# Kernel optimization log

Hardware: AMD Instinct MI355X
Metric: run time of the kernel (lower is better)

Reference implementation:

```python
import jax, jax.numpy as jnp
import numpy as np

HEAD_DIM = 128
N_HEADS = 16
N_KV_HEADS = 4
N_REP = N_HEADS // N_KV_HEADS


def _rope(x, cos, sin):
    # x: [B, S, Hk, D]; cos/sin: [S, D/2]
    xr = x.reshape(*x.shape[:-1], -1, 2)
    x0, x1 = xr[..., 0], xr[..., 1]
    c = cos[None, :, None, :]
    s = sin[None, :, None, :]
    o0 = x0 * c - x1 * s
    o1 = x0 * s + x1 * c
    return jnp.stack([o0, o1], axis=-1).reshape(x.shape)


def setup_inputs() -> dict:
    key = jax.random.key(0)
    ks = jax.random.split(key, 7)
    B, S, DIM = 2, 1024, 2048
    KV_DIM = HEAD_DIM * N_KV_HEADS
    x = jax.random.normal(ks[0], (B, S, DIM), dtype=jnp.float32)
    # rotary angles like LLaMA: freqs = 1/10000^(2i/D)
    inv_freq = 1.0 / (10000.0 ** (np.arange(0, HEAD_DIM, 2, dtype=np.float32) / HEAD_DIM))
    ang = np.arange(S, dtype=np.float32)[:, None] * inv_freq[None, :]  # [S, D/2]
    theta_cos = jnp.asarray(np.cos(ang))
    theta_sin = jnp.asarray(np.sin(ang))
    sc = 0.02
    wq = jax.random.normal(ks[1], (DIM, DIM), dtype=jnp.float32) * sc
    wk = jax.random.normal(ks[2], (DIM, KV_DIM), dtype=jnp.float32) * sc
    wv = jax.random.normal(ks[3], (DIM, KV_DIM), dtype=jnp.float32) * sc
    wo = jax.random.normal(ks[4], (DIM, DIM), dtype=jnp.float32) * sc
    return {"x": x, "theta_cos": theta_cos, "theta_sin": theta_sin,
            "wq": wq, "wk": wk, "wv": wv, "wo": wo}


def reference(x, theta_cos, theta_sin, wq, wk, wv, wo):
    B, S, DIM = x.shape
    # projections
    xq = (x @ wq).reshape(B, S, N_HEADS, HEAD_DIM).transpose(0, 2, 1, 3)  # [B,H,S,D]
    xk = (x @ wk).reshape(B, S, N_KV_HEADS, HEAD_DIM)                      # [B,S,Hk,D]
    xv = (x @ wv).reshape(B, S, N_KV_HEADS, HEAD_DIM)
    # RoPE on K and V only (faithful to source: Q is NOT rotated)
    xk = _rope(xk, theta_cos, theta_sin)
    xv = _rope(xv, theta_cos, theta_sin)
    # GQA repeat: [B,S,Hk,D] -> [B,H,S,D] (each kv head repeated consecutively)
    xk = jnp.repeat(xk.transpose(0, 2, 1, 3), N_REP, axis=1)
    xv = jnp.repeat(xv.transpose(0, 2, 1, 3), N_REP, axis=1)
    scale = HEAD_DIM ** (-0.5)
    att = jnp.einsum('bhqd,bhkd->bhqk', xq, xk) * scale
    # faithful masking: tril then masked_fill(att == 0, -inf)
    tri = jnp.tril(jnp.ones((S, S), dtype=bool))
    att = jnp.where(tri[None, None], att, 0.0)
    att = jnp.where(att == 0.0, -jnp.inf, att)
    att = jax.nn.softmax(att, axis=-1)
    y = jnp.einsum('bhqk,bhkd->bhqd', att, xv)
    out = y.transpose(0, 2, 1, 3).reshape(B, S, DIM)
    return out @ wo
```

## Files before the change

kernel.cpp:

```cpp
#include <hip/hip_runtime.h>
#include <hip/hip_bf16.h>
#include <stdint.h>
#include <math.h>

typedef _Float16 half_t;
typedef __attribute__((ext_vector_type(2))) _Float16 h2_t;
typedef __attribute__((ext_vector_type(4))) _Float16 h4_t;
typedef __attribute__((ext_vector_type(8))) _Float16 h8_t;
typedef __attribute__((ext_vector_type(4))) float f32x4;

#if __has_builtin(__builtin_amdgcn_exp2f)
#define EXP2(x) __builtin_amdgcn_exp2f(x)
#else
#define EXP2(x) exp2f(x)
#endif

__device__ __forceinline__ void gload16(const void* g, void* l) {
    __builtin_amdgcn_global_load_lds(
        (const __attribute__((address_space(1))) uint32_t*)(uintptr_t)g,
        (__attribute__((address_space(3))) uint32_t*)(uint32_t)(uintptr_t)l,
        16, 0, 0);
}

__global__ __launch_bounds__(256) void prep(const float* __restrict__ x, half_t* __restrict__ xh,
                                            const float* __restrict__ wq, const float* __restrict__ wk,
                                            const float* __restrict__ wv, const float* __restrict__ wo,
                                            half_t* __restrict__ qt, half_t* __restrict__ kt,
                                            half_t* __restrict__ vt, half_t* __restrict__ ot) {
    __shared__ half_t T[32][36];
    const int bx = blockIdx.x;
    if (bx < 2048) {
        int g = (bx * 256 + threadIdx.x) * 8;
        float4 a = *(const float4*)(x + g);
        float4 b = *(const float4*)(x + g + 4);
        h8_t o = {(half_t)a.x,(half_t)a.y,(half_t)a.z,(half_t)a.w,
                  (half_t)b.x,(half_t)b.y,(half_t)b.z,(half_t)b.w};
        *(h8_t*)(xh + g) = o;
        return;
    }
    const int wb = bx - 2048;
    const float* src; half_t* dst; int Nd, t;
    if (wb < 4096)      { src = wq; dst = qt; Nd = 2048; t = wb; }
    else if (wb < 5120) { src = wk; dst = kt; Nd = 512;  t = wb - 4096; }
    else if (wb < 6144) { src = wv; dst = vt; Nd = 512;  t = wb - 5120; }
    else                { src = wo; dst = ot; Nd = 2048; t = wb - 6144; }
    const int K = 2048;
    int nt = Nd >> 5;
    int ti = t / nt, tj = t % nt;
    int r  = threadIdx.x >> 3;
    int c4 = (threadIdx.x & 7) << 2;
    float4 v = *(const float4*)(src + (size_t)(ti*32 + r) * Nd + tj*32 + c4);
    T[r][c4+0] = (half_t)v.x; T[r][c4+1] = (half_t)v.y;
    T[r][c4+2] = (half_t)v.z; T[r][c4+3] = (half_t)v.w;
    __syncthreads();
    h4_t o = {T[c4+0][r], T[c4+1][r], T[c4+2][r], T[c4+3][r]};
    *(h4_t*)(dst + (size_t)(tj*32 + r) * K + ti*32 + c4) = o;
}

template<int BM, int QKV, typename CT>
__global__ __launch_bounds__(256) void gemm_t(const half_t* __restrict__ A,
                                              const half_t* __restrict__ Bq,
                                              const half_t* __restrict__ Bk,
                                              const half_t* __restrict__ Bv,
                                              CT* __restrict__ Cq,
                                              half_t* __restrict__ Ck,
                                              half_t* __restrict__ Cv,
                                              int NB, int K) {
    constexpr int MI  = BM / 32;
    constexpr int ACH = BM / 8;
    constexpr int TOT = ACH + 16;
    constexpr int PW  = TOT / 4;
    __shared__ half_t Ah[BM * 64];
    __shared__ half_t Bh[128 * 64];
    const int tid = threadIdx.x, lane = tid & 63, wid = tid >> 6;
    const int lr = lane & 15, lg = lane >> 4;
    const int wm = wid >> 1, wn = wid & 1;
    const int nwg = gridDim.x, bid = blockIdx.x;
    const int swz = (bid & 7) * (nwg >> 3) + (bid >> 3);
    const int bm = swz / NB, bn = swz % NB;
    const int m0 = bm * BM;

    const half_t* W; CT* Cc; int cs, col0;
    if constexpr (QKV) {
        if (bn < 16)      { W = Bq + (size_t)bn * 128 * K;        Cc = Cq;       cs = 2048; col0 = bn * 128; }
        else if (bn < 20) { W = Bk + (size_t)(bn - 16) * 128 * K; Cc = (CT*)Ck;  cs = 512;  col0 = (bn - 16) * 128; }
        else              { W = Bv + (size_t)(bn - 20) * 128 * K; Cc = (CT*)Cv;  cs = 512;  col0 = (bn - 20) * 128; }
    } else {
        W = Bq + (size_t)bn * 128 * K; Cc = Cq; cs = NB * 128; col0 = bn * 128;
    }

    const half_t* Arow = A + (size_t)m0 * K;
    f32x4 acc[MI][4] = {};

    for (int k0 = 0; k0 < K; k0 += 64) {
        #pragma unroll
        for (int c = 0; c < PW; c++) {
            const int chunk = wid * PW + c;
            const int o = lane * 16;
            if (chunk < ACH) {
                const int go   = (chunk << 10) + o;
                const int row  = go >> 7;
                const int colb = (go & 127) ^ ((row & 7) << 4);
                gload16(Arow + (size_t)row * K + k0 + (colb >> 1), (char*)Ah + (chunk << 10));
            } else {
                const int go   = ((chunk - ACH) << 10) + o;
                const int row  = go >> 7;
                const int colb = (go & 127) ^ ((row & 7) << 4);
                gload16(W + (size_t)row * K + k0 + (colb >> 1), (char*)Bh + ((chunk - ACH) << 10));
            }
        }
        __syncthreads();
        h8_t af[2][MI], bf[2][4];
        #pragma unroll
        for (int kk = 0; kk < 2; kk++) {
            #pragma unroll
            for (int mi = 0; mi < MI; mi++) {
                const int row = wm * (BM / 2) + mi * 16 + lr;
                const int cb  = (kk * 64 + lg * 16) ^ ((lr & 7) << 4);
                af[kk][mi] = *(const h8_t*)((const char*)Ah + row * 128 + cb);
            }
            #pragma unroll
            for (int ni = 0; ni < 4; ni++) {
                const int row = wn * 64 + ni * 16 + lr;
                const int cb  = (kk * 64 + lg * 16) ^ ((lr & 7) << 4);
                bf[kk][ni] = *(const h8_t*)((const char*)Bh + row * 128 + cb);
            }
        }
        #pragma unroll
        for (int kk = 0; kk < 2; kk++)
            #pragma unroll
            for (int mi = 0; mi < MI; mi++)
                #pragma unroll
                for (int ni = 0; ni < 4; ni++)
                    acc[mi][ni] = __builtin_amdgcn_mfma_f32_16x16x32_f16(af[kk][mi], bf[kk][ni], acc[mi][ni], 0, 0, 0);
        __syncthreads();
    }

    #pragma unroll
    for (int mi = 0; mi < MI; mi++)
        #pragma unroll
        for (int ni = 0; ni < 4; ni++)
            #pragma unroll
            for (int r = 0; r < 4; r++) {
                int row = m0 + wm * (BM / 2) + mi * 16 + lg * 4 + r;
                int col = col0 + wn * 64 + ni * 16 + lr;
                Cc[(size_t)row * cs + col] = (CT)acc[mi][ni][r];
            }
}

__global__ __launch_bounds__(256) void rope(half_t* __restrict__ Kh, const half_t* __restrict__ Vh,
                                            half_t* __restrict__ Vt, const float* __restrict__ cs,
                                            const float* __restrict__ sn) {
    const int bx = blockIdx.x;
    if (bx < 2048) {
        int gid = bx * 256 + threadIdx.x;
        int row = gid >> 8;
        int pc  = gid & 255;
        int s   = row & 1023;
        int p   = pc & 63;
        float c = cs[s * 64 + p], si = sn[s * 64 + p];
        h2_t v = *(h2_t*)(Kh + (size_t)row * 512 + 2 * pc);
        float x0 = (float)v[0], x1 = (float)v[1];
        h2_t o = {(half_t)(x0 * c - x1 * si), (half_t)(x0 * si + x1 * c)};
        *(h2_t*)(Kh + (size_t)row * 512 + 2 * pc) = o;
        return;
    }
    int gid = (bx - 2048) * 256 + threadIdx.x;
    int col = gid & 2047;
    int dp  = gid >> 11;
    int s   = col & 1023;
    int p   = dp & 63;
    float c = cs[s * 64 + p], si = sn[s * 64 + p];
    h2_t v = *(const h2_t*)(Vh + (size_t)col * 512 + 2 * dp);
    float x0 = (float)v[0], x1 = (float)v[1];
    Vt[(size_t)(2 * dp)     * 2048 + col] = (half_t)(x0 * c - x1 * si);
    Vt[(size_t)(2 * dp + 1) * 2048 + col] = (half_t)(x0 * si + x1 * c);
}

__global__ __launch_bounds__(256, 2) void attn7(const half_t* __restrict__ Qh,
                                                const half_t* __restrict__ Kh,
                                                const half_t* __restrict__ Vtg,
                                                half_t* __restrict__ Yh,
                                                half_t* __restrict__ Yp,
                                                float* __restrict__ ML) {
    __shared__ half_t K0[64 * 128], K1[64 * 128];
    __shared__ half_t V0[128 * 64], V1[128 * 64];
    __shared__ half_t Pl[4][16][72];

    const int tid = threadIdx.x, lane = tid & 63, wid = tid >> 6;
    const int lr = lane & 15, lg = lane >> 4;
    const int bx = blockIdx.x;
    const int g  = bx & 7;
    const int local = bx >> 3;
    const int b = g >> 2, kvh = g & 3;
    const int h = kvh * 4 + (local & 3);
    const int pp = local >> 2;
    int qt, kb0, kb1, part; bool partial;
    if (pp < 8)            { qt = 8 + pp;          kb0 = 0; kb1 = 7;  partial = true;  part = 0; }
    else if (!(pp & 1))    { qt = 7 - ((pp-8)>>1); kb0 = 0; kb1 = qt; partial = false; part = 0; }
    else                   { qt = 15 - ((pp-9)>>1); kb0 = 8; kb1 = qt; partial = true; part = 1; }

    const int qbase = qt * 64 + wid * 16;
    const size_t qrow0 = (size_t)(b * 1024 + qbase);
    const size_t kbase = (size_t)b * 1024;

    const float sc2 = 0.08838834764831845f * 1.4426950408889634f;
    h8_t qf[4];
    #pragma unroll
    for (int kk = 0; kk < 4; kk++) {
        qf[kk] = *(const h8_t*)(Qh + (qrow0 + lr) * 2048 + h * 128 + kk * 32 + lg * 8);
        qf[kk] = qf[kk] * (half_t)sc2;
    }

    float m[4], l[4];
    f32x4 yacc[8] = {};
    #pragma unroll
    for (int r = 0; r < 4; r++) { m[r] = -1e30f; l[r] = 0.f; }

    auto stage = [&](half_t* kt, half_t* vb, int kb) {
        const int j = kb * 64;
        #pragma unroll
        for (int c = 0; c < 4; c++) {
            const int chunk = wid * 4 + c;
            const int o = (chunk << 10) + lane * 16;
            { const int row  = o >> 8;
              const int colb = (o & 255) ^ ((row & 7) << 4);
              gload16(Kh + (kbase + j + row) * 512 + kvh * 128 + (colb >> 1),
                      (char*)kt + (chunk << 10)); }
            { const int row  = o >> 7;
              const int colb = (o & 127) ^ ((row & 7) << 4);
              gload16(Vtg + (size_t)(kvh * 128 + row) * 2048 + kbase + j + (colb >> 1),
                      (char*)vb + (chunk << 10)); }
        }
    };

    auto iter = [&](const half_t* kt, const half_t* vb, int kb) {
        const int j = kb * 64;
        f32x4 st[4] = {};
        #pragma unroll
        for (int t4 = 0; t4 < 4; t4++)
            #pragma unroll
            for (int kk = 0; kk < 4; kk++) {
                const int row = t4 * 16 + lr;
                const int cb  = (kk * 64 + lg * 16) ^ ((lr & 7) << 4);
                h8_t kf = *(const h8_t*)((const char*)kt + row * 256 + cb);
                st[t4] = __builtin_amdgcn_mfma_f32_16x16x32_f16(qf[kk], kf, st[t4], 0, 0, 0);
            }
        if (kb == qt) {
            #pragma unroll
            for (int t4 = 0; t4 < 4; t4++)
                #pragma unroll
                for (int r = 0; r < 4; r++) {
                    int q = qbase + lg * 4 + r;
                    if (j + t4 * 16 + lr > q) st[t4][r] = -1e30f;
                }
        }
        float mb[4];
        #pragma unroll
        for (int r = 0; r < 4; r++)
            mb[r] = fmaxf(fmaxf(st[0][r], st[1][r]), fmaxf(st[2][r], st[3][r]));
        #pragma unroll
        for (int off = 1; off < 16; off <<= 1)
            #pragma unroll
            for (int r = 0; r < 4; r++)
                mb[r] = fmaxf(mb[r], __shfl_xor(mb[r], off));
        float need = 0.f;
        #pragma unroll
        for (int r = 0; r < 4; r++) need = fmaxf(need, mb[r] - m[r]);
        if (!__all(need <= 8.0f)) {
            float al[4];
            #pragma unroll
            for (int r = 0; r < 4; r++) {
                float mn = fmaxf(m[r], mb[r]);
                al[r] = EXP2(m[r] - mn);
                m[r]  = mn;
                l[r] *= al[r];
            }
            #pragma unroll
            for (int dt = 0; dt < 8; dt++)
                #pragma unroll
                for (int r = 0; r < 4; r++)
                    yacc[dt][r] *= al[r];
        }
        float rs[4] = {0.f, 0.f, 0.f, 0.f};
        #pragma unroll
        for (int t4 = 0; t4 < 4; t4++)
            #pragma unroll
            for (int r = 0; r < 4; r++) {
                float p = EXP2(st[t4][r] - m[r]);
                st[t4][r] = p;
                rs[r] += p;
            }
        #pragma unroll
        for (int off = 1; off < 16; off <<= 1)
            #pragma unroll
            for (int r = 0; r < 4; r++)
                rs[r] += __shfl_xor(rs[r], off);
        #pragma unroll
        for (int r = 0; r < 4; r++) l[r] += rs[r];
        #pragma unroll
        for (int t4 = 0; t4 < 4; t4++)
            #pragma unroll
            for (int r = 0; r < 4; r++)
                Pl[wid][lg * 4 + r][t4 * 16 + lr] = (half_t)st[t4][r];
        h8_t pa0 = *(const h8_t*)(&Pl[wid][lr][lg * 8]);
        h8_t pa1 = *(const h8_t*)(&Pl[wid][lr][32 + lg * 8]);
        #pragma unroll
        for (int dt = 0; dt < 8; dt++) {
            const int row = dt * 16 + lr;
            const int cb0 = (lg * 16) ^ ((lr & 7) << 4);
            const int cb1 = (64 + lg * 16) ^ ((lr & 7) << 4);
            h8_t v0 = *(const h8_t*)((const char*)vb + row * 128 + cb0);
            h8_t v1 = *(const h8_t*)((const char*)vb + row * 128 + cb1);
            yacc[dt] = __builtin_amdgcn_mfma_f32_16x16x32_f16(pa0, v0, yacc[dt], 0, 0, 0);
            yacc[dt] = __builtin_amdgcn_mfma_f32_16x16x32_f16(pa1, v1, yacc[dt], 0, 0, 0);
        }
    };

    stage(K0, V0, kb0);
    __syncthreads();
    for (int kb = kb0; kb <= kb1; kb += 2) {
        if (kb + 1 <= kb1) stage(K1, V1, kb + 1);
        iter(K0, V0, kb);
        __syncthreads();
        if (kb + 1 <= kb1) {
            if (kb + 2 <= kb1) stage(K0, V0, kb + 2);
            iter(K1, V1, kb + 1);
            __syncthreads();
        }
    }

    if (!partial) {
        #pragma unroll
        for (int r = 0; r < 4; r++) {
            float inv = 1.0f / l[r];
            #pragma unroll
            for (int dt = 0; dt < 8; dt++)
                Yh[(qrow0 + lg * 4 + r) * 2048 + h * 128 + dt * 16 + lr] =
                    (half_t)(yacc[dt][r] * inv);
        }
    } else {
        const int pidx = ((b * 16 + h) * 8 + (qt - 8)) * 2 + part;
        half_t* yp = Yp + (size_t)pidx * 8192;
        #pragma unroll
        for (int r = 0; r < 4; r++) {
            const int rl = wid * 16 + lg * 4 + r;
            float inv = 1.0f / l[r];
            #pragma unroll
            for (int dt = 0; dt < 8; dt++)
                yp[rl * 128 + dt * 16 + lr] = (half_t)(yacc[dt][r] * inv);
        }
        if (lr == 0) {
            float* ml = ML + (size_t)pidx * 128;
            #pragma unroll
            for (int r = 0; r < 4; r++) {
                const int rl = wid * 16 + lg * 4 + r;
                ml[rl]      = m[r];
                ml[64 + rl] = l[r];
            }
        }
    }
}

__global__ __launch_bounds__(256) void merge2(const half_t* __restrict__ Yp,
                                              const float* __restrict__ ML,
                                              half_t* __restrict__ Yh) {
    const int sidx = blockIdx.x;
    const int b = sidx >> 7;
    const int rem = sidx & 127;
    const int h = rem >> 3;
    const int qt = 8 + (rem & 7);
    const int t = threadIdx.x;
    const int row = t >> 2;
    const int cg = (t & 3) * 32;
    const float* ml0 = ML + (size_t)(sidx * 2) * 128;
    const float* ml1 = ml0 + 128;
    const float m0 = ml0[row], l0 = ml0[64 + row];
    const float m1 = ml1[row], l1 = ml1[64 + row];
    const float M  = fmaxf(m0, m1);
    const float w0 = l0 * EXP2(m0 - M), w1 = l1 * EXP2(m1 - M);
    const float inv = 1.0f / (w0 + w1);
    const float a0 = w0 * inv, a1 = w1 * inv;
    const half_t* y0 = Yp + (size_t)(sidx * 2) * 8192 + row * 128 + cg;
    const half_t* y1 = y0 + 8192;
    half_t* out = Yh + ((size_t)(b * 1024 + qt * 64 + row)) * 2048 + h * 128 + cg;
    #pragma unroll
    for (int c = 0; c < 32; c += 8) {
        h8_t u = *(const h8_t*)(y0 + c);
        h8_t v = *(const h8_t*)(y1 + c);
        h8_t o;
        #pragma unroll
        for (int e = 0; e < 8; e++)
            o[e] = (half_t)(a0 * (float)u[e] + a1 * (float)v[e]);
        *(h8_t*)(out + c) = o;
    }
}

extern "C" void kernel_launch(void* const* d_in, const int* in_sizes, int n_in,
                              void* d_out, int out_size, void* d_ws, size_t ws_size,
                              hipStream_t stream) {
    const float* x  = (const float*)d_in[0];
    const float* tc = (const float*)d_in[1];
    const float* ts = (const float*)d_in[2];
    const float* wq = (const float*)d_in[3];
    const float* wk = (const float*)d_in[4];
    const float* wv = (const float*)d_in[5];
    const float* wo = (const float*)d_in[6];
    float* out = (float*)d_out;

    const size_t MD = 2048ull * 2048, MK = 2048ull * 512;
    half_t* Xh  = (half_t*)d_ws;
    half_t* Qh  = Xh  + MD;
    half_t* Kh  = Qh  + MD;
    half_t* Vh  = Kh  + MK;
    half_t* Vt  = Vh  + MK;
    half_t* Yh  = Vt  + MK;
    half_t* wqt = Yh  + MD;
    half_t* wkt = wqt + MD;
    half_t* wvt = wkt + MK;
    half_t* wot = wvt + MK;
    half_t* Yp  = wot + MD;
    float*  ML  = (float*)(Yp + 512ull * 8192);

    prep<<<12288, 256, 0, stream>>>(x, Xh, wq, wk, wv, wo, wqt, wkt, wvt, wot);
    gemm_t<64, 1, half_t><<<768, 256, 0, stream>>>(Xh, wqt, wkt, wvt, Qh, Kh, Vh, 24, 2048);
    rope<<<4096, 256, 0, stream>>>(Kh, Vh, Vt, tc, ts);
    attn7<<<768, 256, 0, stream>>>(Qh, Kh, Vt, Yh, Yp, ML);
    merge2<<<256, 256, 0, stream>>>(Yp, ML, Yh);
    gemm_t<64, 0, float><<<512, 256, 0, stream>>>(Yh, wot, nullptr, nullptr, out, nullptr, nullptr, 16, 2048);
}
```

Measured before the change: 122.3 us.

## Transpose attention MFMAs, keep P in registers, single-buffer LDS for higher occupancy

The attention kernel swaps the MFMA operand order so each lane holds one query row. That makes softmax row statistics per-lane scalars, needing only two cross-lane shuffles. The P tile is repacked through register shuffles instead of an LDS round trip, and K/V staging drops from double to single buffering so four blocks fit per CU. It also adds s_setprio around the MFMA bursts and vectorised output stores, but loses the overlap of global loads with compute inside a block.

After: 119.4 us. 2.4% less time.

```diff
diff --git a/kernel.cpp b/kernel.cpp
--- a/kernel.cpp
+++ b/kernel.cpp
@@ -8,6 +8,7 @@
 typedef __attribute__((ext_vector_type(4))) _Float16 h4_t;
 typedef __attribute__((ext_vector_type(8))) _Float16 h8_t;
 typedef __attribute__((ext_vector_type(4))) float f32x4;
+typedef __attribute__((ext_vector_type(4))) uint32_t u32x4;
 
 #if __has_builtin(__builtin_amdgcn_exp2f)
 #define EXP2(x) __builtin_amdgcn_exp2f(x)
@@ -177,15 +178,14 @@
     Vt[(size_t)(2 * dp + 1) * 2048 + col] = (half_t)(x0 * si + x1 * c);
 }
 
-__global__ __launch_bounds__(256, 2) void attn7(const half_t* __restrict__ Qh,
+__global__ __launch_bounds__(256, 4) void attn8(const half_t* __restrict__ Qh,
                                                 const half_t* __restrict__ Kh,
                                                 const half_t* __restrict__ Vtg,
                                                 half_t* __restrict__ Yh,
                                                 half_t* __restrict__ Yp,
                                                 float* __restrict__ ML) {
-    __shared__ half_t K0[64 * 128], K1[64 * 128];
-    __shared__ half_t V0[128 * 64], V1[128 * 64];
-    __shared__ half_t Pl[4][16][72];
+    __shared__ half_t K0[64 * 128];
+    __shared__ half_t V0[128 * 64];
 
     const int tid = threadIdx.x, lane = tid & 63, wid = tid >> 6;
     const int lr = lane & 15, lg = lane >> 4;
@@ -196,11 +196,12 @@
     const int h = kvh * 4 + (local & 3);
     const int pp = local >> 2;
     int qt, kb0, kb1, part; bool partial;
-    if (pp < 8)            { qt = 8 + pp;          kb0 = 0; kb1 = 7;  partial = true;  part = 0; }
-    else if (!(pp & 1))    { qt = 7 - ((pp-8)>>1); kb0 = 0; kb1 = qt; partial = false; part = 0; }
-    else                   { qt = 15 - ((pp-9)>>1); kb0 = 8; kb1 = qt; partial = true; part = 1; }
+    if (pp < 8)            { qt = 8 + pp;           kb0 = 0; kb1 = 7;  partial = true;  part = 0; }
+    else if (!(pp & 1))    { qt = 7 - ((pp-8)>>1);  kb0 = 0; kb1 = qt; partial = false; part = 0; }
+    else                   { qt = 15 - ((pp-9)>>1); kb0 = 8; kb1 = qt; partial = true;  part = 1; }
 
     const int qbase = qt * 64 + wid * 16;
+    const int q     = qbase + lr;
     const size_t qrow0 = (size_t)(b * 1024 + qbase);
     const size_t kbase = (size_t)b * 1024;
 
@@ -208,17 +209,16 @@
     h8_t qf[4];
     #pragma unroll
     for (int kk = 0; kk < 4; kk++) {
-        qf[kk] = *(const h8_t*)(Qh + (qrow0 + lr) * 2048 + h * 128 + kk * 32 + lg * 8);
+        qf[kk] = *(const h8_t*)(Qh + ((size_t)(b * 1024) + q) * 2048 + h * 128 + kk * 32 + lg * 8);
         qf[kk] = qf[kk] * (half_t)sc2;
     }
 
-    float m[4], l[4];
+    float m = -1e30f, l = 0.f;
     f32x4 yacc[8] = {};
-    #pragma unroll
-    for (int r = 0; r < 4; r++) { m[r] = -1e30f; l[r] = 0.f; }
-
-    auto stage = [&](half_t* kt, half_t* vb, int kb) {
+
+    for (int kb = kb0; kb <= kb1; kb++) {
         const int j = kb * 64;
+        __syncthreads();
         #pragma unroll
         for (int c = 0; c < 4; c++) {
             const int chunk = wid * 4 + c;
@@ -226,138 +226,124 @@
             { const int row  = o >> 8;
               const int colb = (o & 255) ^ ((row & 7) << 4);
               gload16(Kh + (kbase + j + row) * 512 + kvh * 128 + (colb >> 1),
-                      (char*)kt + (chunk << 10)); }
+                      (char*)K0 + (chunk << 10)); }
             { const int row  = o >> 7;
               const int colb = (o & 127) ^ ((row & 7) << 4);
               gload16(Vtg + (size_t)(kvh * 128 + row) * 2048 + kbase + j + (colb >> 1),
-                      (char*)vb + (chunk << 10)); }
-        }
-    };
-
-    auto iter = [&](const half_t* kt, const half_t* vb, int kb) {
-        const int j = kb * 64;
+                      (char*)V0 + (chunk << 10)); }
+        }
+        __syncthreads();
+
         f32x4 st[4] = {};
+        __builtin_amdgcn_s_setprio(1);
         #pragma unroll
         for (int t4 = 0; t4 < 4; t4++)
             #pragma unroll
             for (int kk = 0; kk < 4; kk++) {
                 const int row = t4 * 16 + lr;
                 const int cb  = (kk * 64 + lg * 16) ^ ((lr & 7) << 4);
-                h8_t kf = *(const h8_t*)((const char*)kt + row * 256 + cb);
-                st[t4] = __builtin_amdgcn_mfma_f32_16x16x32_f16(qf[kk], kf, st[t4], 0, 0, 0);
-            }
+                h8_t kf = *(const h8_t*)((const char*)K0 + row * 256 + cb);
+                st[t4] = __builtin_amdgcn_mfma_f32_16x16x32_f16(kf, qf[kk], st[t4], 0, 0, 0);
+            }
+        __builtin_amdgcn_s_setprio(0);
         if (kb == qt) {
             #pragma unroll
             for (int t4 = 0; t4 < 4; t4++)
                 #pragma unroll
-                for (int r = 0; r < 4; r++) {
-                    int q = qbase + lg * 4 + r;
-                    if (j + t4 * 16 + lr > q) st[t4][r] = -1e30f;
-                }
-        }
-        float mb[4];
-        #pragma unroll
-        for (int r = 0; r < 4; r++)
-            mb[r] = fmaxf(fmaxf(st[0][r], st[1][r]), fmaxf(st[2][r], st[3][r]));
-        #pragma unroll
-        for (int off = 1; off < 16; off <<= 1)
-            #pragma unroll
-            for (int r = 0; r < 4; r++)
-                mb[r] = fmaxf(mb[r], __shfl_xor(mb[r], off));
-        float need = 0.f;
-        #pragma unroll
-        for (int r = 0; r < 4; r++) need = fmaxf(need, mb[r] - m[r]);
-        if (!__all(need <= 8.0f)) {
-            float al[4];
-            #pragma unroll
-            for (int r = 0; r < 4; r++) {
-                float mn = fmaxf(m[r], mb[r]);
-                al[r] = EXP2(m[r] - mn);
-                m[r]  = mn;
-                l[r] *= al[r];
-            }
+                for (int r = 0; r < 4; r++)
+                    if (j + t4 * 16 + lg * 4 + r > q) st[t4][r] = -1e30f;
+        }
+        float mb = fmaxf(fmaxf(fmaxf(st[0][0], st[0][1]), fmaxf(st[0][2], st[0][3])),
+                         fmaxf(fmaxf(st[1][0], st[1][1]), fmaxf(st[1][2], st[1][3])));
+        mb = fmaxf(mb, fmaxf(fmaxf(fmaxf(st[2][0], st[2][1]), fmaxf(st[2][2], st[2][3])),
+                             fmaxf(fmaxf(st[3][0], st[3][1]), fmaxf(st[3][2], st[3][3]))));
+        mb = fmaxf(mb, __shfl_xor(mb, 16));
+        mb = fmaxf(mb, __shfl_xor(mb, 32));
+        if (!__all(mb - m <= 8.0f)) {
+            float mn = fmaxf(m, mb);
+            float al = EXP2(m - mn);
+            m = mn;
+            l *= al;
             #pragma unroll
             for (int dt = 0; dt < 8; dt++)
                 #pragma unroll
                 for (int r = 0; r < 4; r++)
-                    yacc[dt][r] *= al[r];
-        }
-        float rs[4] = {0.f, 0.f, 0.f, 0.f};
+                    yacc[dt][r] *= al;
+        }
+        float rs = 0.f;
         #pragma unroll
         for (int t4 = 0; t4 < 4; t4++)
             #pragma unroll
             for (int r = 0; r < 4; r++) {
-                float p = EXP2(st[t4][r] - m[r]);
+                float p = EXP2(st[t4][r] - m);
                 st[t4][r] = p;
-                rs[r] += p;
-            }
-        #pragma unroll
-        for (int off = 1; off < 16; off <<= 1)
-            #pragma unroll
-            for (int r = 0; r < 4; r++)
-                rs[r] += __shfl_xor(rs[r], off);
-        #pragma unroll
-        for (int r = 0; r < 4; r++) l[r] += rs[r];
-        #pragma unroll
-        for (int t4 = 0; t4 < 4; t4++)
-            #pragma unroll
-            for (int r = 0; r < 4; r++)
-                Pl[wid][lg * 4 + r][t4 * 16 + lr] = (half_t)st[t4][r];
-        h8_t pa0 = *(const h8_t*)(&Pl[wid][lr][lg * 8]);
-        h8_t pa1 = *(const h8_t*)(&Pl[wid][lr][32 + lg * 8]);
+                rs += p;
+            }
+        rs += __shfl_xor(rs, 16);
+        rs += __shfl_xor(rs, 32);
+        l += rs;
+        uint32_t h2p[4][2];
+        #pragma unroll
+        for (int t4 = 0; t4 < 4; t4++) {
+            h2p[t4][0] = __builtin_bit_cast(uint32_t,
+                __builtin_amdgcn_cvt_pkrtz(st[t4][0], st[t4][1]));
+            h2p[t4][1] = __builtin_bit_cast(uint32_t,
+                __builtin_amdgcn_cvt_pkrtz(st[t4][2], st[t4][3]));
+        }
+        const int src1 = ((lg & 1) << 5) + lr;
+        const int src2 = src1 + 16;
+        const bool sel = (lg < 2);
+        h8_t pb[2];
+        #pragma unroll
+        for (int c = 0; c < 2; c++) {
+            uint32_t lo0 = __shfl((int)h2p[2*c][0],   src1);
+            uint32_t lo1 = __shfl((int)h2p[2*c][1],   src1);
+            uint32_t lo2 = __shfl((int)h2p[2*c][0],   src2);
+            uint32_t lo3 = __shfl((int)h2p[2*c][1],   src2);
+            uint32_t hi0 = __shfl((int)h2p[2*c+1][0], src1);
+            uint32_t hi1 = __shfl((int)h2p[2*c+1][1], src1);
+            uint32_t hi2 = __shfl((int)h2p[2*c+1][0], src2);
+            uint32_t hi3 = __shfl((int)h2p[2*c+1][1], src2);
+            u32x4 w = { sel ? lo0 : hi0, sel ? lo1 : hi1,
+                        sel ? lo2 : hi2, sel ? lo3 : hi3 };
+            pb[c] = __builtin_bit_cast(h8_t, w);
+        }
+        __builtin_amdgcn_s_setprio(1);
         #pragma unroll
         for (int dt = 0; dt < 8; dt++) {
             const int row = dt * 16 + lr;
             const int cb0 = (lg * 16) ^ ((lr & 7) << 4);
             const int cb1 = (64 + lg * 16) ^ ((lr & 7) << 4);
-            h8_t v0 = *(const h8_t*)((const char*)vb + row * 128 + cb0);
-            h8_t v1 = *(const h8_t*)((const char*)vb + row * 128 + cb1);
-            yacc[dt] = __builtin_amdgcn_mfma_f32_16x16x32_f16(pa0, v0, yacc[dt], 0, 0, 0);
-            yacc[dt] = __builtin_amdgcn_mfma_f32_16x16x32_f16(pa1, v1, yacc[dt], 0, 0, 0);
-        }
-    };
-
-    stage(K0, V0, kb0);
-    __syncthreads();
-    for (int kb = kb0; kb <= kb1; kb += 2) {
-        if (kb + 1 <= kb1) stage(K1, V1, kb + 1);
-        iter(K0, V0, kb);
-        __syncthreads();
-        if (kb + 1 <= kb1) {
-            if (kb + 2 <= kb1) stage(K0, V0, kb + 2);
-            iter(K1, V1, kb + 1);
-            __syncthreads();
-        }
-    }
-
+            h8_t v0 = *(const h8_t*)((const char*)V0 + row * 128 + cb0);
+            h8_t v1 = *(const h8_t*)((const char*)V0 + row * 128 + cb1);
+            yacc[dt] = __builtin_amdgcn_mfma_f32_16x16x32_f16(v0, pb[0], yacc[dt], 0, 0, 0);
+            yacc[dt] = __builtin_amdgcn_mfma_f32_16x16x32_f16(v1, pb[1], yacc[dt], 0, 0, 0);
+        }
+        __builtin_amdgcn_s_setprio(0);
+    }
+
+    const float inv = 1.0f / l;
     if (!partial) {
         #pragma unroll
-        for (int r = 0; r < 4; r++) {
-            float inv = 1.0f / l[r];
-            #pragma unroll
-            for (int dt = 0; dt < 8; dt++)
-                Yh[(qrow0 + lg * 4 + r) * 2048 + h * 128 + dt * 16 + lr] =
-                    (half_t)(yacc[dt][r] * inv);
+        for (int dt = 0; dt < 8; dt++) {
+            h4_t o = {(half_t)(yacc[dt][0] * inv), (half_t)(yacc[dt][1] * inv),
+                      (half_t)(yacc[dt][2] * inv), (half_t)(yacc[dt][3] * inv)};
+            *(h4_t*)(Yh + ((size_t)(b * 1024) + q) * 2048 + h * 128 + dt * 16 + lg * 4) = o;
         }
     } else {
         const int pidx = ((b * 16 + h) * 8 + (qt - 8)) * 2 + part;
         half_t* yp = Yp + (size_t)pidx * 8192;
-        #pragma unroll
-        for (int r = 0; r < 4; r++) {
-            const int rl = wid * 16 + lg * 4 + r;
-            float inv = 1.0f / l[r];
-            #pragma unroll
-            for (int dt = 0; dt < 8; dt++)
-                yp[rl * 128 + dt * 16 + lr] = (half_t)(yacc[dt][r] * inv);
-        }
-        if (lr == 0) {
+        const int rl = wid * 16 + lr;
+        #pragma unroll
+        for (int dt = 0; dt < 8; dt++) {
+            h4_t o = {(half_t)(yacc[dt][0] * inv), (half_t)(yacc[dt][1] * inv),
+                      (half_t)(yacc[dt][2] * inv), (half_t)(yacc[dt][3] * inv)};
+            *(h4_t*)(yp + rl * 128 + dt * 16 + lg * 4) = o;
+        }
+        if (lg == 0) {
             float* ml = ML + (size_t)pidx * 128;
-            #pragma unroll
-            for (int r = 0; r < 4; r++) {
-                const int rl = wid * 16 + lg * 4 + r;
-                ml[rl]      = m[r];
-                ml[64 + rl] = l[r];
-            }
+            ml[rl]      = m;
+            ml[64 + rl] = l;
         }
     }
 }
@@ -425,7 +411,7 @@
     prep<<<12288, 256, 0, stream>>>(x, Xh, wq, wk, wv, wo, wqt, wkt, wvt, wot);
     gemm_t<64, 1, half_t><<<768, 256, 0, stream>>>(Xh, wqt, wkt, wvt, Qh, Kh, Vh, 24, 2048);
     rope<<<4096, 256, 0, stream>>>(Kh, Vh, Vt, tc, ts);
-    attn7<<<768, 256, 0, stream>>>(Qh, Kh, Vt, Yh, Yp, ML);
+    attn8<<<768, 256, 0, stream>>>(Qh, Kh, Vt, Yh, Yp, ML);
     merge2<<<256, 256, 0, stream>>>(Yp, ML, Yh);
     gemm_t<64, 0, float><<<512, 256, 0, stream>>>(Yh, wot, nullptr, nullptr, out, nullptr, nullptr, 16, 2048);
 }
```
